# Kernel optimization log

Hardware: AMD Instinct MI355X
Metric: run time of the kernel (lower is better)

## Reference

```python
import jax, jax.numpy as jnp
import numpy as np

B, T, D = 8, 2048, 1024
GAMMA = 0.96875


def setup_inputs() -> dict:
    key = jax.random.key(0)
    ks = jax.random.split(key, 7)
    sD = 1.0 / np.sqrt(D)
    sT = 1.0 / np.sqrt(T)
    return {
        "x": jax.random.normal(ks[0], (B, T, D), dtype=jnp.float32),
        "Wq": jax.random.normal(ks[1], (D, D), dtype=jnp.float32) * sD,
        "Wk": jax.random.normal(ks[2], (D, D), dtype=jnp.float32) * sD,
        "Wv": jax.random.normal(ks[3], (D, D), dtype=jnp.float32) * sD,
        "W_ih": jax.random.normal(ks[4], (T, T), dtype=jnp.float32) * sT,
        "W_hh": jax.random.normal(ks[5], (T, T), dtype=jnp.float32) * sT,
        "b_ih": jax.random.normal(ks[6], (T,), dtype=jnp.float32) * sT,
    }


def reference(x, Wq, Wk, Wv, W_ih, W_hh, b_ih):
    # x: [B, T, D]; QKV projections (Linear with no bias: x @ W^T)
    Q = jnp.einsum("btd,ed->bte", x, Wq)
    K = jnp.einsum("btd,ed->bte", x, Wk)
    V = jnp.einsum("btd,ed->bte", x, Wv)

    # retention state injected as hidden bias of the tanh-RNN: [B, T]
    bias = jnp.sum(K * V, axis=-1)

    gamma = jnp.full((T,), GAMMA, dtype=x.dtype)
    u = gamma @ W_ih.T + b_ih  # input contribution, identical every step: [T]

    def step(h, b_t):
        h_new = jnp.tanh(u + h @ W_hh.T + b_t)
        return h_new, h_new

    h0 = jnp.zeros((T,), dtype=x.dtype)
    _, S = jax.lax.scan(step, h0, bias)  # scan over the B rows -> S: [B, T]

    # vmap(mul)(S, Q^T)^T  ==  out[b,t,d] = S[b,t] * Q[b,t,d]
    return S[:, :, None] * Q
```

## Files before the change

kernel.cpp:

```cpp
#include <hip/hip_runtime.h>
#include <stdint.h>

#define T_DIM 2048
#define D_DIM 1024
#define B_DIM 8
#define M_TOK (B_DIM * T_DIM)
#define GAMMA_C 0.96875f

typedef float f32x4 __attribute__((ext_vector_type(4)));
typedef float f32x16 __attribute__((ext_vector_type(16)));
typedef float fl4 __attribute__((ext_vector_type(4)));
typedef __bf16 bf16x8 __attribute__((ext_vector_type(8)));
typedef unsigned short us8 __attribute__((ext_vector_type(8)));
typedef unsigned short us4 __attribute__((ext_vector_type(4)));

__device__ __forceinline__ unsigned short f32_bf16_rne(float f) {
  uint32_t u = __builtin_bit_cast(uint32_t, f);
  return (unsigned short)((u + 0x7FFFu + ((u >> 16) & 1u)) >> 16);
}
__device__ __forceinline__ float bf16_f32(unsigned short h) {
  uint32_t u = ((uint32_t)h) << 16;
  return __builtin_bit_cast(float, u);
}

__device__ __forceinline__ int swz_row(int r) {
  return ((r >> 1) & 3) ^ ((r >> 3) & 3);
}

__device__ __forceinline__ void gload16(const void* g, void* l) {
  __builtin_amdgcn_global_load_lds(
      reinterpret_cast<const __attribute__((address_space(1))) uint32_t*>(
          reinterpret_cast<uintptr_t>(g)),
      reinterpret_cast<__attribute__((address_space(3))) uint32_t*>(
          reinterpret_cast<uintptr_t>(l)),
      16, 0, 0);
}

__device__ __forceinline__ bf16x8 ldfrag(const unsigned short* p) {
  us8 u = *reinterpret_cast<const us8*>(p);
  return __builtin_bit_cast(bf16x8, u);
}

#define VMW(n) asm volatile("s_waitcnt vmcnt(" #n ")" ::: "memory")
#define BAR    __builtin_amdgcn_s_barrier()

__global__ __launch_bounds__(256) void k_split(const float* __restrict__ in, int n8,
                                               unsigned short* __restrict__ hi,
                                               unsigned short* __restrict__ lo) {
  int stride = gridDim.x * blockDim.x;
  for (int i = blockIdx.x * blockDim.x + threadIdx.x; i < n8; i += stride) {
    fl4 v0 = ((const fl4*)in)[i * 2];
    fl4 v1 = ((const fl4*)in)[i * 2 + 1];
    us8 h, l;
#pragma unroll
    for (int j = 0; j < 4; ++j) {
      unsigned short hb = f32_bf16_rne(v0[j]);
      h[j] = hb;
      l[j] = f32_bf16_rne(v0[j] - bf16_f32(hb));
      unsigned short hb1 = f32_bf16_rne(v1[j]);
      h[j + 4] = hb1;
      l[j + 4] = f32_bf16_rne(v1[j] - bf16_f32(hb1));
    }
    ((us8*)hi)[i] = h;
    ((us8*)lo)[i] = l;
  }
}

__global__ __launch_bounds__(256) void k_split_hi(const float* __restrict__ in, int n8,
                                                  unsigned short* __restrict__ hi) {
  int stride = gridDim.x * blockDim.x;
  for (int i = blockIdx.x * blockDim.x + threadIdx.x; i < n8; i += stride) {
    fl4 v0 = ((const fl4*)in)[i * 2];
    fl4 v1 = ((const fl4*)in)[i * 2 + 1];
    us8 h;
#pragma unroll
    for (int j = 0; j < 4; ++j) {
      h[j] = f32_bf16_rne(v0[j]);
      h[j + 4] = f32_bf16_rne(v1[j]);
    }
    ((us8*)hi)[i] = h;
  }
}

__global__ __launch_bounds__(256) void k_split_T(const float* __restrict__ in,
                                                 unsigned short* __restrict__ th,
                                                 unsigned short* __restrict__ tl) {
  __shared__ float tile[64][69];
  int be = blockIdx.x >> 4, bd = blockIdx.x & 15;
  int e0 = be * 64, d0 = bd * 64;
  int r = threadIdx.x >> 4;
  int c = (threadIdx.x & 15) * 4;
#pragma unroll
  for (int it = 0; it < 4; ++it) {
    int rr = r + it * 16;
    fl4 v = *(const fl4*)(in + (size_t)(e0 + rr) * D_DIM + d0 + c);
#pragma unroll
    for (int j = 0; j < 4; ++j) tile[rr][c + j] = v[j];
  }
  __syncthreads();
#pragma unroll
  for (int it = 0; it < 4; ++it) {
    int dr = r + it * 16;
    us4 h, l;
#pragma unroll
    for (int j = 0; j < 4; ++j) {
      float f = tile[c + j][dr];
      h[j] = f32_bf16_rne(f);
      l[j] = f32_bf16_rne(f - bf16_f32(h[j]));
    }
    *(us4*)(th + (size_t)(d0 + dr) * D_DIM + e0 + c) = h;
    *(us4*)(tl + (size_t)(d0 + dr) * D_DIM + e0 + c) = l;
  }
}

__global__ __launch_bounds__(256) void k_u(const float* __restrict__ Wih,
                                           const float* __restrict__ bih,
                                           float* __restrict__ u) {
  int wave = threadIdx.x >> 6, lane = threadIdx.x & 63;
  int t = blockIdx.x * 4 + wave;
  const fl4* row = (const fl4*)(Wih + (size_t)t * T_DIM);
  float s = 0.f;
#pragma unroll
  for (int i = 0; i < 8; ++i) {
    fl4 v = row[lane + i * 64];
    s += v[0] + v[1] + v[2] + v[3];
  }
#pragma unroll
  for (int m = 32; m >= 1; m >>= 1) s += __shfl_xor(s, m, 64);
  if (lane == 0) u[t] = GAMMA_C * s + bih[t];
}

__global__ __launch_bounds__(256) void k_step_bf(const unsigned short* __restrict__ Whh_b,
                                                 const float* __restrict__ hprev,
                                                 const float* __restrict__ u,
                                                 const float* __restrict__ biasrow,
                                                 float* __restrict__ hout) {
  int wave = threadIdx.x >> 6, lane = threadIdx.x & 63;
  int t = blockIdx.x * 4 + wave;
  const unsigned short* row = Whh_b + (size_t)t * T_DIM;
  float s = 0.f;
#pragma unroll
  for (int i = 0; i < 4; ++i) {
    us8 w = *(const us8*)(row + i * 512 + lane * 8);
    fl4 h0 = *(const fl4*)(hprev + i * 512 + lane * 8);
    fl4 h1 = *(const fl4*)(hprev + i * 512 + lane * 8 + 4);
    s += bf16_f32(w[0]) * h0[0] + bf16_f32(w[1]) * h0[1] +
         bf16_f32(w[2]) * h0[2] + bf16_f32(w[3]) * h0[3] +
         bf16_f32(w[4]) * h1[0] + bf16_f32(w[5]) * h1[1] +
         bf16_f32(w[6]) * h1[2] + bf16_f32(w[7]) * h1[3];
  }
#pragma unroll
  for (int m = 32; m >= 1; m >>= 1) s += __shfl_xor(s, m, 64);
  if (lane == 0) hout[t] = tanhf(u[t] + s + biasrow[t]);
}

__global__ __launch_bounds__(256) void k_ht(
    const unsigned short* __restrict__ ah, const unsigned short* __restrict__ al,
    const unsigned short* __restrict__ bh, const unsigned short* __restrict__ bl,
    float* __restrict__ Hf) {
  __shared__ unsigned short sAh[2][64 * 32], sAl[2][64 * 32];
  __shared__ unsigned short sBh[2][64 * 32], sBl[2][64 * 32];
  const int tid = threadIdx.x;
  const int wave = tid >> 6, lane = tid & 63;
  const int wm = wave >> 1, wn = wave & 1;
  const int m0 = (blockIdx.x >> 4) * 64, n0 = (blockIdx.x & 15) * 64;
  const int hi32 = lane >> 5;

  const int srow = tid >> 2;
  const int csrc = (tid & 3) ^ swz_row(srow);
  const size_t ga = (size_t)(m0 + srow) * D_DIM + csrc * 8;
  const size_t gb = (size_t)(n0 + srow) * D_DIM + csrc * 8;
  const int ldst = tid * 8;

  f32x16 acc = {};
  const int l31 = lane & 31;
  const int sw = swz_row(l31);
  const int ar = wm * 32 + l31;
  const int br = wn * 32 + l31;
  int aoff[2], boff[2];
#pragma unroll
  for (int kh = 0; kh < 2; ++kh) {
    aoff[kh] = ar * 32 + (((kh * 2 + hi32) ^ sw) * 8);
    boff[kh] = br * 32 + (((kh * 2 + hi32) ^ sw) * 8);
  }

  auto stage = [&](int t, int buf) {
    const size_t ko = (size_t)t * 32;
    gload16(ah + ga + ko, &sAh[buf][ldst]);
    gload16(al + ga + ko, &sAl[buf][ldst]);
    gload16(bh + gb + ko, &sBh[buf][ldst]);
    gload16(bl + gb + ko, &sBl[buf][ldst]);
  };

  stage(0, 0);
  stage(1, 1);
  for (int kt = 0; kt < 32; ++kt) {
    const int cur = kt & 1;
    if (kt < 31) { VMW(4); } else { VMW(0); }
    BAR;
#pragma unroll
    for (int kh = 0; kh < 2; ++kh) {
      bf16x8 fah = ldfrag(&sAh[cur][aoff[kh]]);
      bf16x8 fal = ldfrag(&sAl[cur][aoff[kh]]);
      bf16x8 fbh = ldfrag(&sBh[cur][boff[kh]]);
      bf16x8 fbl = ldfrag(&sBl[cur][boff[kh]]);
      acc = __builtin_amdgcn_mfma_f32_32x32x16_bf16(fah, fbh, acc, 0, 0, 0);
      acc = __builtin_amdgcn_mfma_f32_32x32x16_bf16(fah, fbl, acc, 0, 0, 0);
      acc = __builtin_amdgcn_mfma_f32_32x32x16_bf16(fal, fbh, acc, 0, 0, 0);
    }
    BAR;
    if (kt + 2 <= 31) stage(kt + 2, cur);
  }
#pragma unroll
  for (int r = 0; r < 16; ++r) {
    int row = m0 + wm * 32 + (r & 3) + 8 * (r >> 2) + 4 * hi32;
    int col = n0 + wn * 32 + l31;
    Hf[(size_t)row * D_DIM + col] = acc[r];
  }
}

__global__ __launch_bounds__(256) void k_nprime(const float* __restrict__ Hf,
                                                unsigned short* __restrict__ mh,
                                                unsigned short* __restrict__ ml) {
  __shared__ float t2[64][65];
  const int ti = blockIdx.x >> 4;
  const int tj = blockIdx.x & 15;
  const int r0 = ti * 64, c0 = tj * 64;
  const int a = threadIdx.x >> 2;
  const int b4 = (threadIdx.x & 3) * 16;
  if (tj < ti) {
#pragma unroll
    for (int j = 0; j < 16; ++j) {
      size_t ad = (size_t)(r0 + a) * D_DIM + c0 + b4 + j;
      mh[ad] = 0;
      ml[ad] = 0;
    }
    return;
  }
#pragma unroll
  for (int j = 0; j < 16; j += 4) {
    fl4 v = *(const fl4*)(Hf + (size_t)(c0 + a) * D_DIM + r0 + b4 + j);
#pragma unroll
    for (int q = 0; q < 4; ++q) t2[a][b4 + j + q] = v[q];
  }
  __syncthreads();
#pragma unroll
  for (int j = 0; j < 16; ++j) {
    int dp = r0 + a;
    int dd = c0 + b4 + j;
    float v = 0.f;
    if (dd > dp)       v = Hf[(size_t)dp * D_DIM + dd] + t2[b4 + j][a];
    else if (dd == dp) v = Hf[(size_t)dp * D_DIM + dd];
    unsigned short hb = f32_bf16_rne(v);
    unsigned short lb = f32_bf16_rne(v - bf16_f32(hb));
    size_t ad = (size_t)dp * D_DIM + dd;
    mh[ad] = hb;
    ml[ad] = lb;
  }
}

__global__ __launch_bounds__(512, 2) void k_y_bias(
    const unsigned short* __restrict__ xh, const unsigned short* __restrict__ xl,
    const unsigned short* __restrict__ bh, const unsigned short* __restrict__ bl,
    float* __restrict__ bias) {
  __shared__ unsigned short sAh[3][128 * 32], sAl[3][128 * 32];
  __shared__ unsigned short sBh[3][128 * 32], sBl[3][128 * 32];
  const int tid = threadIdx.x;
  const int wave = tid >> 6, lane = tid & 63;
  const int wm = wave >> 2, wn = wave & 3;
  const int xcd = blockIdx.x & 7, seq = blockIdx.x >> 3;
  const int mb = xcd * 16 + (seq >> 2);
  const int np = seq & 3;
  const int m0 = mb * 128;
  const int hi32 = lane >> 5;
  const int l31 = lane & 31;

  const int srow = tid >> 2;
  const int csrc = (tid & 3) ^ swz_row(srow);
  const size_t gA = (size_t)(m0 + srow) * D_DIM + csrc * 8;
  const int ldst = tid * 8;

  int aoff[2][2], boff[2];
#pragma unroll
  for (int mi = 0; mi < 2; ++mi) {
    int r = wm * 64 + mi * 32 + l31;
    int sw = swz_row(r);
#pragma unroll
    for (int kh = 0; kh < 2; ++kh)
      aoff[mi][kh] = r * 32 + (((kh * 2 + hi32) ^ sw) * 8);
  }
  {
    int r = wn * 32 + l31;
    int sw = swz_row(r);
#pragma unroll
    for (int kh = 0; kh < 2; ++kh)
      boff[kh] = r * 32 + (((kh * 2 + hi32) ^ sw) * 8);
  }

  auto phase = [&](int nb) {
    const int n0 = nb * 128;
    const int k0 = nb * 4, ke = 32;
    const size_t gB = (size_t)(n0 + srow) * D_DIM + csrc * 8;

    auto stage = [&](int t, int buf) {
      const size_t ko = (size_t)t * 32;
      gload16(xh + gA + ko, &sAh[buf][ldst]);
      gload16(xl + gA + ko, &sAl[buf][ldst]);
      gload16(bh + gB + ko, &sBh[buf][ldst]);
      gload16(bl + gB + ko, &sBl[buf][ldst]);
    };

    f32x16 acc[2] = {};
    BAR;
    stage(k0, 0);
    stage(k0 + 1, 1);
    int cur = 0;
    for (int kt = k0; kt < ke; ++kt) {
      if (kt < ke - 1) { VMW(4); } else { VMW(0); }
      BAR;
      int nx = cur + 2; if (nx >= 3) nx -= 3;
      if (kt + 2 < ke) stage(kt + 2, nx);
#pragma unroll
      for (int kh = 0; kh < 2; ++kh) {
        bf16x8 fah[2], fal[2];
#pragma unroll
        for (int mi = 0; mi < 2; ++mi) {
          fah[mi] = ldfrag(&sAh[cur][aoff[mi][kh]]);
          fal[mi] = ldfrag(&sAl[cur][aoff[mi][kh]]);
        }
        bf16x8 fbh = ldfrag(&sBh[cur][boff[kh]]);
        bf16x8 fbl = ldfrag(&sBl[cur][boff[kh]]);
        __builtin_amdgcn_s_setprio(1);
#pragma unroll
        for (int mi = 0; mi < 2; ++mi) {
          acc[mi] = __builtin_amdgcn_mfma_f32_32x32x16_bf16(fah[mi], fbh, acc[mi], 0, 0, 0);
          acc[mi] = __builtin_amdgcn_mfma_f32_32x32x16_bf16(fah[mi], fbl, acc[mi], 0, 0, 0);
          acc[mi] = __builtin_amdgcn_mfma_f32_32x32x16_bf16(fal[mi], fbh, acc[mi], 0, 0, 0);
        }
        __builtin_amdgcn_s_setprio(0);
      }
      cur = cur + 1; if (cur >= 3) cur -= 3;
    }

#pragma unroll
    for (int mi = 0; mi < 2; ++mi)
#pragma unroll
      for (int r = 0; r < 16; ++r) {
        int row = m0 + wm * 64 + mi * 32 + (r & 3) + 8 * (r >> 2) + 4 * hi32;
        size_t ix = (size_t)row * D_DIM + n0 + wn * 32 + l31;
        float xv = bf16_f32(xh[ix]) + bf16_f32(xl[ix]);
        float p = xv * acc[mi][r];
        p += __shfl_xor(p, 1, 64);
        p += __shfl_xor(p, 2, 64);
        p += __shfl_xor(p, 4, 64);
        p += __shfl_xor(p, 8, 64);
        p += __shfl_xor(p, 16, 64);
        if (l31 == 0) atomicAdd(&bias[row], p);
      }
  };

  phase(np);
  phase(7 - np);
}

__global__ __launch_bounds__(256, 4) void k_q_out(
    const unsigned short* __restrict__ xh,
    const unsigned short* __restrict__ qh_,
    const float* __restrict__ S, float* __restrict__ out) {
  __shared__ unsigned short sA[2][128 * 32];
  __shared__ unsigned short sB[2][128 * 32];
  const int tid = threadIdx.x;
  const int wave = tid >> 6, lane = tid & 63;
  const int wm = wave >> 1, wn = wave & 1;
  int sw0 = (blockIdx.x & 7) * 128 + (blockIdx.x >> 3);
  const int mb = sw0 >> 3, nb = sw0 & 7;
  const int m0 = mb * 128, n0 = nb * 128;
  const int hi32 = lane >> 5;
  const int l31 = lane & 31;

  const int srow0 = tid >> 2, srow1 = srow0 + 64;
  const int csrc0 = (tid & 3) ^ swz_row(srow0);
  const int csrc1 = (tid & 3) ^ swz_row(srow1);
  const size_t gaA0 = (size_t)(m0 + srow0) * D_DIM + csrc0 * 8;
  const size_t gaA1 = (size_t)(m0 + srow1) * D_DIM + csrc1 * 8;
  const size_t gaB0 = (size_t)(n0 + srow0) * D_DIM + csrc0 * 8;
  const size_t gaB1 = (size_t)(n0 + srow1) * D_DIM + csrc1 * 8;
  const int ldst0 = tid * 8, ldst1 = (tid + 256) * 8;

  f32x16 acc[2][2] = {};
  int aoff[2][2], boff[2][2];
#pragma unroll
  for (int mi = 0; mi < 2; ++mi) {
    int r = wm * 64 + mi * 32 + l31;
    int sw = swz_row(r);
#pragma unroll
    for (int kh = 0; kh < 2; ++kh)
      aoff[mi][kh] = r * 32 + (((kh * 2 + hi32) ^ sw) * 8);
  }
#pragma unroll
  for (int ni = 0; ni < 2; ++ni) {
    int r = wn * 64 + ni * 32 + l31;
    int sw = swz_row(r);
#pragma unroll
    for (int kh = 0; kh < 2; ++kh)
      boff[ni][kh] = r * 32 + (((kh * 2 + hi32) ^ sw) * 8);
  }

  auto stage = [&](int t, int buf) {
    const size_t ko = (size_t)t * 32;
    gload16(xh + gaA0 + ko, &sA[buf][ldst0]);
    gload16(xh + gaA1 + ko, &sA[buf][ldst1]);
    gload16(qh_ + gaB0 + ko, &sB[buf][ldst0]);
    gload16(qh_ + gaB1 + ko, &sB[buf][ldst1]);
  };

  stage(0, 0);
  stage(1, 1);
  for (int kt = 0; kt < 32; ++kt) {
    const int cur = kt & 1;
    if (kt < 31) { VMW(4); } else { VMW(0); }
    BAR;
#pragma unroll
    for (int kh = 0; kh < 2; ++kh) {
      bf16x8 fa[2], fb[2];
#pragma unroll
      for (int mi = 0; mi < 2; ++mi) fa[mi] = ldfrag(&sA[cur][aoff[mi][kh]]);
#pragma unroll
      for (int ni = 0; ni < 2; ++ni) fb[ni] = ldfrag(&sB[cur][boff[ni][kh]]);
      __builtin_amdgcn_s_setprio(1);
#pragma unroll
      for (int mi = 0; mi < 2; ++mi)
#pragma unroll
        for (int ni = 0; ni < 2; ++ni)
          acc[mi][ni] = __builtin_amdgcn_mfma_f32_32x32x16_bf16(fa[mi], fb[ni], acc[mi][ni], 0, 0, 0);
      __builtin_amdgcn_s_setprio(0);
    }
    BAR;
    if (kt + 2 <= 31) stage(kt + 2, cur);
  }

#pragma unroll
  for (int mi = 0; mi < 2; ++mi)
#pragma unroll
    for (int r = 0; r < 16; ++r) {
      int row = m0 + wm * 64 + mi * 32 + (r & 3) + 8 * (r >> 2) + 4 * hi32;
      float sc = S[row];
      float* orow = out + (size_t)row * D_DIM + n0 + wn * 64 + l31;
      orow[0] = sc * acc[mi][0][r];
      orow[32] = sc * acc[mi][1][r];
    }
}

extern "C" void kernel_launch(void* const* d_in, const int* in_sizes, int n_in,
                              void* d_out, int out_size, void* d_ws, size_t ws_size,
                              hipStream_t stream) {
  const float* x   = (const float*)d_in[0];
  const float* Wq  = (const float*)d_in[1];
  const float* Wk  = (const float*)d_in[2];
  const float* Wv  = (const float*)d_in[3];
  const float* Wih = (const float*)d_in[4];
  const float* Whh = (const float*)d_in[5];
  const float* bih = (const float*)d_in[6];
  float* out = (float*)d_out;

  char* ws = (char*)d_ws;
  size_t off = 0;
  auto alloc = [&](size_t bytes) -> char* {
    char* p = ws + off;
    off += (bytes + 255) & ~(size_t)255;
    return p;
  };
  unsigned short* xh   = (unsigned short*)alloc((size_t)M_TOK * D_DIM * 2);
  unsigned short* xl   = (unsigned short*)alloc((size_t)M_TOK * D_DIM * 2);
  unsigned short* wqh  = (unsigned short*)alloc((size_t)D_DIM * D_DIM * 2);
  unsigned short* wkth = (unsigned short*)alloc((size_t)D_DIM * D_DIM * 2);
  unsigned short* wktl = (unsigned short*)alloc((size_t)D_DIM * D_DIM * 2);
  unsigned short* wvth = (unsigned short*)alloc((size_t)D_DIM * D_DIM * 2);
  unsigned short* wvtl = (unsigned short*)alloc((size_t)D_DIM * D_DIM * 2);
  unsigned short* mph  = (unsigned short*)alloc((size_t)D_DIM * D_DIM * 2);
  unsigned short* mpl  = (unsigned short*)alloc((size_t)D_DIM * D_DIM * 2);
  float* Hf   = (float*)alloc((size_t)D_DIM * D_DIM * 4);
  float* bias = (float*)alloc((size_t)M_TOK * 4);
  float* Sbuf = (float*)alloc((size_t)M_TOK * 4);
  float* ubuf = (float*)alloc((size_t)T_DIM * 4);
  float* zbuf = (float*)alloc((size_t)T_DIM * 4);
  unsigned short* whhb = wkth;
  (void)ws_size; (void)in_sizes; (void)n_in; (void)out_size;

  k_split<<<2048, 256, 0, stream>>>(x, M_TOK * D_DIM / 8, xh, xl);
  k_split_hi<<<512, 256, 0, stream>>>(Wq, D_DIM * D_DIM / 8, wqh);
  k_split_T<<<256, 256, 0, stream>>>(Wk, wkth, wktl);
  k_split_T<<<256, 256, 0, stream>>>(Wv, wvth, wvtl);

  hipMemsetAsync(bias, 0, (size_t)M_TOK * 4, stream);
  hipMemsetAsync(zbuf, 0, (size_t)T_DIM * 4, stream);

  k_u<<<T_DIM / 4, 256, 0, stream>>>(Wih, bih, ubuf);

  k_ht<<<256, 256, 0, stream>>>(wvth, wvtl, wkth, wktl, Hf);

  k_nprime<<<256, 256, 0, stream>>>(Hf, mph, mpl);

  k_split_hi<<<1024, 256, 0, stream>>>(Whh, T_DIM * T_DIM / 8, whhb);

  k_y_bias<<<512, 512, 0, stream>>>(xh, xl, mph, mpl, bias);

  for (int b = 0; b < B_DIM; ++b) {
    const float* hp = (b == 0) ? zbuf : (Sbuf + (size_t)(b - 1) * T_DIM);
    k_step_bf<<<T_DIM / 4, 256, 0, stream>>>(whhb, hp, ubuf, bias + (size_t)b * T_DIM,
                                             Sbuf + (size_t)b * T_DIM);
  }

  k_q_out<<<1024, 256, 0, stream>>>(xh, wqh, Sbuf, out);
}
```

Measured before the change: 267.9 us.

## Widen bias GEMM tile to 128x256 with 16x16x32 MFMA and rebalance triangular work

Restructures the k_y_bias kernel that computes the quadratic-form bias over a triangular matrix: the N tile grows from 128 to 256 columns, each wave computes a 64x64 sub-tile with 16x16x32 MFMAs instead of 32x32x16, and the grid halves to 256 blocks. The triangular work is split into two halves with explicit k-ranges per phase so both block types get similar work. The aim is more reuse of A fragments per LDS load and less x reloading. In exchange it needs more LDS and registers (acc becomes 16 f32x4 tiles), which may lower occupancy.

```diff
diff --git a/kernel.cpp b/kernel.cpp
--- a/kernel.cpp
+++ b/kernel.cpp
@@ -264,103 +264,115 @@
     const unsigned short* __restrict__ bh, const unsigned short* __restrict__ bl,
     float* __restrict__ bias) {
   __shared__ unsigned short sAh[3][128 * 32], sAl[3][128 * 32];
-  __shared__ unsigned short sBh[3][128 * 32], sBl[3][128 * 32];
+  __shared__ unsigned short sBh[3][256 * 32], sBl[3][256 * 32];
   const int tid = threadIdx.x;
   const int wave = tid >> 6, lane = tid & 63;
-  const int wm = wave >> 2, wn = wave & 3;
+  const int wm = wave >> 2;
+  const int wn = wave & 3;
   const int xcd = blockIdx.x & 7, seq = blockIdx.x >> 3;
-  const int mb = xcd * 16 + (seq >> 2);
-  const int np = seq & 3;
+  const int mb = xcd * 16 + (seq >> 1);
+  const int half = seq & 1;
   const int m0 = mb * 128;
-  const int hi32 = lane >> 5;
-  const int l31 = lane & 31;
+  const int l15 = lane & 15;
+  const int kc = lane >> 4;
 
   const int srow = tid >> 2;
   const int csrc = (tid & 3) ^ swz_row(srow);
   const size_t gA = (size_t)(m0 + srow) * D_DIM + csrc * 8;
-  const int ldst = tid * 8;
-
-  int aoff[2][2], boff[2];
-#pragma unroll
-  for (int mi = 0; mi < 2; ++mi) {
-    int r = wm * 64 + mi * 32 + l31;
-    int sw = swz_row(r);
-#pragma unroll
-    for (int kh = 0; kh < 2; ++kh)
-      aoff[mi][kh] = r * 32 + (((kh * 2 + hi32) ^ sw) * 8);
-  }
-  {
-    int r = wn * 32 + l31;
-    int sw = swz_row(r);
-#pragma unroll
-    for (int kh = 0; kh < 2; ++kh)
-      boff[kh] = r * 32 + (((kh * 2 + hi32) ^ sw) * 8);
-  }
-
-  auto phase = [&](int nb) {
-    const int n0 = nb * 128;
-    const int k0 = nb * 4, ke = 32;
-    const size_t gB = (size_t)(n0 + srow) * D_DIM + csrc * 8;
+  const int ldstA = tid * 8;
+  const int ldstB0 = tid * 8, ldstB1 = (tid + 512) * 8;
+
+  int aoff[4], boff[4];
+#pragma unroll
+  for (int mi = 0; mi < 4; ++mi) {
+    int r = wm * 64 + mi * 16 + l15;
+    aoff[mi] = r * 32 + ((kc ^ swz_row(r)) * 8);
+  }
+#pragma unroll
+  for (int ni = 0; ni < 4; ++ni) {
+    int r = wn * 64 + ni * 16 + l15;
+    boff[ni] = r * 32 + ((kc ^ swz_row(r)) * 8);
+  }
+
+  auto phase = [&](int nb, int k0, int ke) {
+    const int n0 = nb * 256;
+    const size_t gB0 = (size_t)(n0 + srow) * D_DIM + csrc * 8;
+    const size_t gB1 = (size_t)(n0 + srow + 128) * D_DIM + csrc * 8;
 
     auto stage = [&](int t, int buf) {
       const size_t ko = (size_t)t * 32;
-      gload16(xh + gA + ko, &sAh[buf][ldst]);
-      gload16(xl + gA + ko, &sAl[buf][ldst]);
-      gload16(bh + gB + ko, &sBh[buf][ldst]);
-      gload16(bl + gB + ko, &sBl[buf][ldst]);
+      gload16(xh + gA + ko, &sAh[buf][ldstA]);
+      gload16(xl + gA + ko, &sAl[buf][ldstA]);
+      gload16(bh + gB0 + ko, &sBh[buf][ldstB0]);
+      gload16(bh + gB1 + ko, &sBh[buf][ldstB1]);
+      gload16(bl + gB0 + ko, &sBl[buf][ldstB0]);
+      gload16(bl + gB1 + ko, &sBl[buf][ldstB1]);
     };
 
-    f32x16 acc[2] = {};
+    f32x4 acc[4][4] = {};
     BAR;
     stage(k0, 0);
     stage(k0 + 1, 1);
     int cur = 0;
     for (int kt = k0; kt < ke; ++kt) {
-      if (kt < ke - 1) { VMW(4); } else { VMW(0); }
+      if (kt < ke - 1) { VMW(6); } else { VMW(0); }
       BAR;
       int nx = cur + 2; if (nx >= 3) nx -= 3;
       if (kt + 2 < ke) stage(kt + 2, nx);
-#pragma unroll
-      for (int kh = 0; kh < 2; ++kh) {
-        bf16x8 fah[2], fal[2];
-#pragma unroll
-        for (int mi = 0; mi < 2; ++mi) {
-          fah[mi] = ldfrag(&sAh[cur][aoff[mi][kh]]);
-          fal[mi] = ldfrag(&sAl[cur][aoff[mi][kh]]);
+      {
+        bf16x8 fah[4], fal[4], fbh_[4], fbl_[4];
+#pragma unroll
+        for (int mi = 0; mi < 4; ++mi) {
+          fah[mi] = ldfrag(&sAh[cur][aoff[mi]]);
+          fal[mi] = ldfrag(&sAl[cur][aoff[mi]]);
         }
-        bf16x8 fbh = ldfrag(&sBh[cur][boff[kh]]);
-        bf16x8 fbl = ldfrag(&sBl[cur][boff[kh]]);
+#pragma unroll
+        for (int ni = 0; ni < 4; ++ni) {
+          fbh_[ni] = ldfrag(&sBh[cur][boff[ni]]);
+          fbl_[ni] = ldfrag(&sBl[cur][boff[ni]]);
+        }
         __builtin_amdgcn_s_setprio(1);
 #pragma unroll
-        for (int mi = 0; mi < 2; ++mi) {
-          acc[mi] = __builtin_amdgcn_mfma_f32_32x32x16_bf16(fah[mi], fbh, acc[mi], 0, 0, 0);
-          acc[mi] = __builtin_amdgcn_mfma_f32_32x32x16_bf16(fah[mi], fbl, acc[mi], 0, 0, 0);
-          acc[mi] = __builtin_amdgcn_mfma_f32_32x32x16_bf16(fal[mi], fbh, acc[mi], 0, 0, 0);
-        }
+        for (int mi = 0; mi < 4; ++mi)
+#pragma unroll
+          for (int ni = 0; ni < 4; ++ni) {
+            acc[mi][ni] = __builtin_amdgcn_mfma_f32_16x16x32_bf16(fah[mi], fbh_[ni], acc[mi][ni], 0, 0, 0);
+            acc[mi][ni] = __builtin_amdgcn_mfma_f32_16x16x32_bf16(fah[mi], fbl_[ni], acc[mi][ni], 0, 0, 0);
+            acc[mi][ni] = __builtin_amdgcn_mfma_f32_16x16x32_bf16(fal[mi], fbh_[ni], acc[mi][ni], 0, 0, 0);
+          }
         __builtin_amdgcn_s_setprio(0);
       }
       cur = cur + 1; if (cur >= 3) cur -= 3;
     }
 
 #pragma unroll
-    for (int mi = 0; mi < 2; ++mi)
-#pragma unroll
-      for (int r = 0; r < 16; ++r) {
-        int row = m0 + wm * 64 + mi * 32 + (r & 3) + 8 * (r >> 2) + 4 * hi32;
-        size_t ix = (size_t)row * D_DIM + n0 + wn * 32 + l31;
-        float xv = bf16_f32(xh[ix]) + bf16_f32(xl[ix]);
-        float p = xv * acc[mi][r];
+    for (int mi = 0; mi < 4; ++mi)
+#pragma unroll
+      for (int j = 0; j < 4; ++j) {
+        int row = m0 + wm * 64 + mi * 16 + (lane >> 4) * 4 + j;
+        const size_t rb = (size_t)row * D_DIM + n0 + wn * 64 + l15;
+        float p = 0.f;
+#pragma unroll
+        for (int ni = 0; ni < 4; ++ni) {
+          float xv = bf16_f32(xh[rb + ni * 16]) + bf16_f32(xl[rb + ni * 16]);
+          p += xv * acc[mi][ni][j];
+        }
         p += __shfl_xor(p, 1, 64);
         p += __shfl_xor(p, 2, 64);
         p += __shfl_xor(p, 4, 64);
         p += __shfl_xor(p, 8, 64);
-        p += __shfl_xor(p, 16, 64);
-        if (l31 == 0) atomicAdd(&bias[row], p);
+        if (l15 == 0) atomicAdd(&bias[row], p);
       }
   };
 
-  phase(np);
-  phase(7 - np);
+  if (half == 0) {
+    phase(0, 0, 32);
+    phase(1, 8, 16);
+  } else {
+    phase(1, 16, 32);
+    phase(2, 16, 32);
+    phase(3, 24, 32);
+  }
 }
 
 __global__ __launch_bounds__(256, 4) void k_q_out(
@@ -503,7 +515,7 @@
 
   k_split_hi<<<1024, 256, 0, stream>>>(Whh, T_DIM * T_DIM / 8, whhb);
 
-  k_y_bias<<<512, 512, 0, stream>>>(xh, xl, mph, mpl, bias);
+  k_y_bias<<<256, 512, 0, stream>>>(xh, xl, mph, mpl, bias);
 
   for (int b = 0; b < B_DIM; ++b) {
     const float* hp = (b == 0) ? zbuf : (Sbuf + (size_t)(b - 1) * T_DIM);
```

After: 244.5 us. -8.7%, faster.
